# Kernel tuning notes

Measured on AMD Instinct MI355X. Metric: run time of the kernel, lower is better.

The kernel has to match this reference:

```python
import jax, jax.numpy as jnp
import numpy as np

ALPHA = 2.0   # ATan surrogate sharpness (spikingjelly default)
V_TH = 1.0    # spike threshold

@jax.custom_vjp
def spike(v):
    # Heaviside spike at threshold V_TH
    return (v >= V_TH).astype(v.dtype)

def _spike_fwd(v):
    return spike(v), v

def _spike_bwd(v, g):
    # ATan surrogate gradient
    sg = (ALPHA / 2.0) / (1.0 + (jnp.pi / 2.0 * ALPHA * (v - V_TH)) ** 2)
    return (g * sg,)

spike.defvjp(_spike_fwd, _spike_bwd)

N, T, D_IN, HID, D_OUT = 512, 1000, 128, 128, 20

def _linear_params(k, fan_in, fan_out):
    # matches torch nn.Linear default init: U(-1/sqrt(fan_in), 1/sqrt(fan_in))
    s = 1.0 / np.sqrt(fan_in)
    kw, kb = jax.random.split(k)
    W = jax.random.uniform(kw, (fan_out, fan_in), minval=-s, maxval=s, dtype=jnp.float32)
    b = jax.random.uniform(kb, (fan_out,), minval=-s, maxval=s, dtype=jnp.float32)
    return W, b

def setup_inputs() -> dict:
    key = jax.random.key(0)
    kx, k1, k2, k3, k4, k5 = jax.random.split(key, 6)
    x = jax.random.normal(kx, (N, T, D_IN), dtype=jnp.float32)
    Wi1, bi1 = _linear_params(k1, D_IN, HID)   # i2h_1
    Wh1, bh1 = _linear_params(k2, HID, HID)    # h2h_1
    Wi2, bi2 = _linear_params(k3, HID, HID)    # i2h_2
    Wh2, bh2 = _linear_params(k4, HID, HID)    # h2h_2
    Wo,  bo  = _linear_params(k5, HID, D_OUT)  # h2o_2
    return {"x": x, "Wi1": Wi1, "bi1": bi1, "Wh1": Wh1, "bh1": bh1,
            "Wi2": Wi2, "bi2": bi2, "Wh2": Wh2, "bh2": bh2, "Wo": Wo, "bo": bo}

def reference(x, Wi1, bi1, Wh1, bh1, Wi2, bi2, Wh2, bh2, Wo, bo):
    n, t = x.shape[0], x.shape[1]
    s1_0 = jnp.zeros((n, Wh1.shape[0]), dtype=x.dtype)
    s2_0 = jnp.zeros((n, Wh2.shape[0]), dtype=x.dtype)
    acc0 = jnp.zeros((n, Wo.shape[0]), dtype=x.dtype)

    def step(carry, xt):
        s1, s2, acc = carry
        h1 = xt @ Wi1.T + bi1 + s1 @ Wh1.T + bh1
        s1 = spike(h1)
        h2 = s1 @ Wi2.T + bi2 + s2 @ Wh2.T + bh2
        s2 = spike(h2)
        acc = acc + s2 @ Wo.T + bo
        return (s1, s2, acc), None

    # scan over time: x -> [T, N, D_IN]
    (_, _, acc), _ = jax.lax.scan(step, (s1_0, s2_0, acc0), jnp.swapaxes(x, 0, 1))
    return acc / t
```

## Files before the change

### kernel.cpp

```cpp
#include <hip/hip_runtime.h>
#include <cstdint>
#include <cstddef>

#define T_STEPS 1000
#define NS      512
#define HID     128
#define DOUT    20
#define XPAD    129
#define WPAD    129

extern "C" __global__ void __launch_bounds__(512, 1)
srnn_dense(const float* __restrict__ x, const float* __restrict__ Wi1,
           float* __restrict__ D, int t0, int Tc)
{
    extern __shared__ float sm[];
    float* xs = sm;
    float* Wl = sm + 128 * XPAD;
    const int tid = threadIdx.x;
    const int w = tid >> 6, ln = tid & 63;
    const int rb = blockIdx.x * 128;

    for (int i = tid; i < HID * HID / 4; i += 512)
        ((float4*)Wl)[i] = ((const float4*)Wi1)[i];
    for (int i = tid; i < 128 * 32; i += 512) {
        int r = i >> 5, kq = i & 31;
        int cr = rb + r;
        int s = cr / Tc, trel = cr - s * Tc;
        float4 v = ((const float4*)x)[((size_t)s * T_STEPS + t0 + trel) * 32 + kq];
        float* dst = &xs[r * XPAD + 4 * kq];
        dst[0] = v.x; dst[1] = v.y; dst[2] = v.z; dst[3] = v.w;
    }
    __syncthreads();

    const float* xr0 = xs + ln * XPAD;
    const float* xr1 = xs + (64 + ln) * XPAD;
    for (int og = 0; og < 4; ++og) {
        const int o = 16 * w + 4 * og;
        float a[2][4][4];
        #pragma unroll
        for (int r = 0; r < 2; ++r)
            #pragma unroll
            for (int j = 0; j < 4; ++j)
                #pragma unroll
                for (int i = 0; i < 4; ++i) a[r][j][i] = 0.f;

        #pragma unroll 4
        for (int k = 0; k < HID; k += 4) {
            float4 wv[4];
            #pragma unroll
            for (int j = 0; j < 4; ++j)
                wv[j] = *(const float4*)&Wl[(o + j) * HID + k];
            float xa0[4], xa1[4];
            #pragma unroll
            for (int i = 0; i < 4; ++i) { xa0[i] = xr0[k + i]; xa1[i] = xr1[k + i]; }
            #pragma unroll
            for (int j = 0; j < 4; ++j) {
                a[0][j][0] = fmaf(xa0[0], wv[j].x, a[0][j][0]);
                a[0][j][1] = fmaf(xa0[1], wv[j].y, a[0][j][1]);
                a[0][j][2] = fmaf(xa0[2], wv[j].z, a[0][j][2]);
                a[0][j][3] = fmaf(xa0[3], wv[j].w, a[0][j][3]);
                a[1][j][0] = fmaf(xa1[0], wv[j].x, a[1][j][0]);
                a[1][j][1] = fmaf(xa1[1], wv[j].y, a[1][j][1]);
                a[1][j][2] = fmaf(xa1[2], wv[j].z, a[1][j][2]);
                a[1][j][3] = fmaf(xa1[3], wv[j].w, a[1][j][3]);
            }
        }
        #pragma unroll
        for (int r = 0; r < 2; ++r) {
            float4 dv;
            dv.x = (a[r][0][0] + a[r][0][1]) + (a[r][0][2] + a[r][0][3]);
            dv.y = (a[r][1][0] + a[r][1][1]) + (a[r][1][2] + a[r][1][3]);
            dv.z = (a[r][2][0] + a[r][2][1]) + (a[r][2][2] + a[r][2][3]);
            dv.w = (a[r][3][0] + a[r][3][1]) + (a[r][3][2] + a[r][3][3]);
            *(float4*)&D[(size_t)(rb + 64 * r + ln) * HID + o] = dv;
        }
    }
}

extern "C" __global__ void __launch_bounds__(128, 1)
srnn_layer1(const float* __restrict__ D, const float* __restrict__ Wh1,
            const float* __restrict__ bi1, const float* __restrict__ bh1,
            ulonglong2* __restrict__ masks, ulonglong2* __restrict__ state,
            int t0, int Tc, int first)
{
    extern __shared__ float WT[];
    const int tid = threadIdx.x, w = tid >> 6, ln = tid & 63;
    const int s = 2 * blockIdx.x + w;

    for (int i = tid; i < HID * HID / 4; i += 128) {
        int o = i >> 5, jq = i & 31;
        float4 v = ((const float4*)Wh1)[i];
        WT[(4 * jq + 0) * WPAD + o] = v.x; WT[(4 * jq + 1) * WPAD + o] = v.y;
        WT[(4 * jq + 2) * WPAD + o] = v.z; WT[(4 * jq + 3) * WPAD + o] = v.w;
    }
    const float bil = bi1[ln], bih = bi1[64 + ln];
    const float bhl = bh1[ln], bhh = bh1[64 + ln];
    unsigned long long m0 = 0ULL, m1 = 0ULL;
    if (!first) { ulonglong2 st = state[s]; m0 = st.x; m1 = st.y; }

    const float* Drow = D + (size_t)s * Tc * HID;
    float dl[8], dh[8];
    #pragma unroll
    for (int p = 0; p < 8; ++p) {
        int ti = p < Tc ? p : Tc - 1;
        dl[p] = Drow[ti * HID + ln];
        dh[p] = Drow[ti * HID + 64 + ln];
    }
    __syncthreads();

    for (int tt = 0; tt < Tc; tt += 8) {
        #pragma unroll
        for (int u = 0; u < 8; ++u) {
            int t = tt + u;
            if (t >= Tc) break;
            float dense_l = dl[u], dense_h = dh[u];
            int tp = (t + 8 < Tc) ? t + 8 : Tc - 1;
            dl[u] = Drow[tp * HID + ln];
            dh[u] = Drow[tp * HID + 64 + ln];

            float rl = 0.f, rh = 0.f;
            unsigned long long mm = m0;
            while (mm) { int j = __builtin_ctzll(mm); mm &= mm - 1;
                rl += WT[j * WPAD + ln]; rh += WT[j * WPAD + 64 + ln]; }
            mm = m1;
            while (mm) { int j = 64 + __builtin_ctzll(mm); mm &= mm - 1;
                rl += WT[j * WPAD + ln]; rh += WT[j * WPAD + 64 + ln]; }

            float hl = ((dense_l + bil) + rl) + bhl;
            float hh = ((dense_h + bih) + rh) + bhh;
            m0 = __ballot(hl >= 1.0f);
            m1 = __ballot(hh >= 1.0f);
            if (ln == 0) {
                ulonglong2 mv; mv.x = m0; mv.y = m1;
                masks[(size_t)s * T_STEPS + (t0 + t)] = mv;
            }
        }
    }
    if (ln == 0) { ulonglong2 st; st.x = m0; st.y = m1; state[s] = st; }
}

extern "C" __global__ void __launch_bounds__(128, 1)
srnn_layer2(const ulonglong2* __restrict__ masks,
            const float* __restrict__ Wi2, const float* __restrict__ bi2,
            const float* __restrict__ Wh2, const float* __restrict__ bh2,
            const float* __restrict__ Wo,  const float* __restrict__ bo,
            float* __restrict__ out)
{
    extern __shared__ float sm2[];
    float* WI  = sm2;
    float* WH  = sm2 + HID * WPAD;
    float* WOt = sm2 + 2 * HID * WPAD;
    const int tid = threadIdx.x, w = tid >> 6, ln = tid & 63;
    const int s = 2 * blockIdx.x + w;

    for (int i = tid; i < HID * HID / 4; i += 128) {
        int o = i >> 5, jq = i & 31;
        float4 a = ((const float4*)Wi2)[i];
        WI[(4 * jq + 0) * WPAD + o] = a.x; WI[(4 * jq + 1) * WPAD + o] = a.y;
        WI[(4 * jq + 2) * WPAD + o] = a.z; WI[(4 * jq + 3) * WPAD + o] = a.w;
        float4 b = ((const float4*)Wh2)[i];
        WH[(4 * jq + 0) * WPAD + o] = b.x; WH[(4 * jq + 1) * WPAD + o] = b.y;
        WH[(4 * jq + 2) * WPAD + o] = b.z; WH[(4 * jq + 3) * WPAD + o] = b.w;
    }
    for (int i = tid; i < DOUT * HID / 4; i += 128) {
        int o = i >> 5, jq = i & 31;
        float4 v = ((const float4*)Wo)[i];
        WOt[(4 * jq + 0) * DOUT + o] = v.x; WOt[(4 * jq + 1) * DOUT + o] = v.y;
        WOt[(4 * jq + 2) * DOUT + o] = v.z; WOt[(4 * jq + 3) * DOUT + o] = v.w;
    }
    const float bil = bi2[ln], bih = bi2[64 + ln];
    const float bhl = bh2[ln], bhh = bh2[64 + ln];
    const bool  oth = (ln < DOUT);
    const float bol = oth ? bo[ln] : 0.f;

    const ulonglong2* mrow = masks + (size_t)s * T_STEPS;
    ulonglong2 mb[8];
    #pragma unroll
    for (int p = 0; p < 8; ++p) mb[p] = mrow[p];
    unsigned long long p0 = 0ULL, p1 = 0ULL;
    float acc = 0.f;
    __syncthreads();

    for (int tt = 0; tt < T_STEPS; tt += 8) {
        #pragma unroll
        for (int u = 0; u < 8; ++u) {
            int t = tt + u;
            ulonglong2 s1 = mb[u];
            int tp = (t + 8 < T_STEPS) ? t + 8 : T_STEPS - 1;
            mb[u] = mrow[tp];

            float Al = 0.f, Ah = 0.f;
            unsigned long long mm = s1.x;
            while (mm) { int j = __builtin_ctzll(mm); mm &= mm - 1;
                Al += WI[j * WPAD + ln]; Ah += WI[j * WPAD + 64 + ln]; }
            mm = s1.y;
            while (mm) { int j = 64 + __builtin_ctzll(mm); mm &= mm - 1;
                Al += WI[j * WPAD + ln]; Ah += WI[j * WPAD + 64 + ln]; }

            float Bl = 0.f, Bh = 0.f;
            mm = p0;
            while (mm) { int j = __builtin_ctzll(mm); mm &= mm - 1;
                Bl += WH[j * WPAD + ln]; Bh += WH[j * WPAD + 64 + ln]; }
            mm = p1;
            while (mm) { int j = 64 + __builtin_ctzll(mm); mm &= mm - 1;
                Bl += WH[j * WPAD + ln]; Bh += WH[j * WPAD + 64 + ln]; }

            float hl = ((Al + bil) + Bl) + bhl;
            float hh = ((Ah + bih) + Bh) + bhh;
            p0 = __ballot(hl >= 1.0f);
            p1 = __ballot(hh >= 1.0f);

            if (oth) {
                float d = 0.f;
                unsigned long long q = p0;
                while (q) { int j = __builtin_ctzll(q); q &= q - 1; d += WOt[j * DOUT + ln]; }
                q = p1;
                while (q) { int j = 64 + __builtin_ctzll(q); q &= q - 1; d += WOt[j * DOUT + ln]; }
                acc += d;
                acc += bol;
            }
        }
    }
    if (oth) out[s * DOUT + ln] = acc / (float)T_STEPS;
}

extern "C" void kernel_launch(void* const* d_in, const int* in_sizes, int n_in,
                              void* d_out, int out_size, void* d_ws, size_t ws_size,
                              hipStream_t stream) {
    const float* x   = (const float*)d_in[0];
    const float* Wi1 = (const float*)d_in[1];
    const float* bi1 = (const float*)d_in[2];
    const float* Wh1 = (const float*)d_in[3];
    const float* bh1 = (const float*)d_in[4];
    const float* Wi2 = (const float*)d_in[5];
    const float* bi2 = (const float*)d_in[6];
    const float* Wh2 = (const float*)d_in[7];
    const float* bh2 = (const float*)d_in[8];
    const float* Wo  = (const float*)d_in[9];
    const float* bo  = (const float*)d_in[10];
    float* out = (float*)d_out;

    const size_t mask_bytes  = (size_t)NS * T_STEPS * sizeof(ulonglong2);
    const size_t state_bytes = (size_t)NS * sizeof(ulonglong2);
    ulonglong2* masks = (ulonglong2*)d_ws;
    ulonglong2* state = (ulonglong2*)((char*)d_ws + mask_bytes);
    float* D = (float*)((char*)d_ws + mask_bytes + state_bytes);

    size_t avail = ws_size > mask_bytes + state_bytes
                 ? ws_size - mask_bytes - state_bytes : 0;
    const size_t bytes_per_t = (size_t)NS * HID * sizeof(float);
    long tcmax = (long)(avail / bytes_per_t);
    static const int divs[] = {1000, 500, 250, 200, 125, 100, 50, 40, 25, 20, 10, 8, 5, 4, 2, 1};
    int Tc = 1;
    for (int i = 0; i < 16; ++i) if (divs[i] <= tcmax) { Tc = divs[i]; break; }

    const int lds0 = (128 * XPAD + HID * HID) * (int)sizeof(float);
    const int lds1 = (HID * WPAD) * (int)sizeof(float);
    const int lds2 = (2 * HID * WPAD + HID * DOUT) * (int)sizeof(float);
    hipFuncSetAttribute((const void*)srnn_dense,
                        hipFuncAttributeMaxDynamicSharedMemorySize, lds0);
    hipFuncSetAttribute((const void*)srnn_layer1,
                        hipFuncAttributeMaxDynamicSharedMemorySize, lds1);
    hipFuncSetAttribute((const void*)srnn_layer2,
                        hipFuncAttributeMaxDynamicSharedMemorySize, lds2);

    for (int t0 = 0; t0 < T_STEPS; t0 += Tc) {
        srnn_dense<<<4 * Tc, 512, lds0, stream>>>(x, Wi1, D, t0, Tc);
        srnn_layer1<<<NS / 2, 128, lds1, stream>>>(D, Wh1, bi1, bh1, masks, state,
                                                   t0, Tc, t0 == 0 ? 1 : 0);
    }
    srnn_layer2<<<NS / 2, 128, lds2, stream>>>(masks, Wi2, bi2, Wh2, bh2, Wo, bo, out);
}
```

Baseline: 1.766 ms.

## Split layer 2 into parallel sparse input projection, shared recurrence, and output reduction

The serial layer-2 kernel, which did the input projection, recurrence and output dot per time step, is broken into stages. The non-recurrent input projection from layer-1 spikes is computed in parallel across all time steps (srnn_spmm). The layer-1 recurrence kernel is reused for layer 2, and output dots are computed in parallel with a final reduction kernel. The sparse gather loop is also unrolled by four with a zero padding row so that LDS loads can be issued together. This takes non-recurrent work off the sequential critical path, at the cost of extra kernel launches and a larger workspace for masks and dots.

```diff
diff --git a/kernel.cpp b/kernel.cpp
--- a/kernel.cpp
+++ b/kernel.cpp
@@ -77,11 +77,29 @@
     }
 }
 
+__device__ __forceinline__ void sparse4(const float* __restrict__ WT,
+                                        unsigned long long mm, int base,
+                                        int ln, float& rl, float& rh)
+{
+    while (mm) {
+        int j0 = (int)__builtin_ctzll(mm) + base;      mm &= mm - 1;
+        int j1 = mm ? (int)__builtin_ctzll(mm) + base : 128; mm &= mm - 1;
+        int j2 = mm ? (int)__builtin_ctzll(mm) + base : 128; mm &= mm - 1;
+        int j3 = mm ? (int)__builtin_ctzll(mm) + base : 128; mm &= mm - 1;
+        float a0 = WT[j0 * WPAD + ln],      a1 = WT[j1 * WPAD + ln];
+        float a2 = WT[j2 * WPAD + ln],      a3 = WT[j3 * WPAD + ln];
+        float b0 = WT[j0 * WPAD + 64 + ln], b1 = WT[j1 * WPAD + 64 + ln];
+        float b2 = WT[j2 * WPAD + 64 + ln], b3 = WT[j3 * WPAD + 64 + ln];
+        rl += a0; rl += a1; rl += a2; rl += a3;
+        rh += b0; rh += b1; rh += b2; rh += b3;
+    }
+}
+
 extern "C" __global__ void __launch_bounds__(128, 1)
-srnn_layer1(const float* __restrict__ D, const float* __restrict__ Wh1,
-            const float* __restrict__ bi1, const float* __restrict__ bh1,
-            ulonglong2* __restrict__ masks, ulonglong2* __restrict__ state,
-            int t0, int Tc, int first)
+srnn_recur(const float* __restrict__ Dn, const float* __restrict__ Wh,
+           const float* __restrict__ bi, const float* __restrict__ bh,
+           ulonglong2* __restrict__ masks, ulonglong2* __restrict__ state,
+           int t0, int Tc, int first)
 {
     extern __shared__ float WT[];
     const int tid = threadIdx.x, w = tid >> 6, ln = tid & 63;
@@ -89,16 +107,18 @@
 
     for (int i = tid; i < HID * HID / 4; i += 128) {
         int o = i >> 5, jq = i & 31;
-        float4 v = ((const float4*)Wh1)[i];
+        float4 v = ((const float4*)Wh)[i];
         WT[(4 * jq + 0) * WPAD + o] = v.x; WT[(4 * jq + 1) * WPAD + o] = v.y;
         WT[(4 * jq + 2) * WPAD + o] = v.z; WT[(4 * jq + 3) * WPAD + o] = v.w;
     }
-    const float bil = bi1[ln], bih = bi1[64 + ln];
-    const float bhl = bh1[ln], bhh = bh1[64 + ln];
+    for (int i = tid; i < WPAD; i += 128) WT[128 * WPAD + i] = 0.f;
+
+    const float bil = bi[ln], bih = bi[64 + ln];
+    const float bhl = bh[ln], bhh = bh[64 + ln];
     unsigned long long m0 = 0ULL, m1 = 0ULL;
     if (!first) { ulonglong2 st = state[s]; m0 = st.x; m1 = st.y; }
 
-    const float* Drow = D + (size_t)s * Tc * HID;
+    const float* Drow = Dn + (size_t)s * Tc * HID;
     float dl[8], dh[8];
     #pragma unroll
     for (int p = 0; p < 8; ++p) {
@@ -119,12 +139,8 @@
             dh[u] = Drow[tp * HID + 64 + ln];
 
             float rl = 0.f, rh = 0.f;
-            unsigned long long mm = m0;
-            while (mm) { int j = __builtin_ctzll(mm); mm &= mm - 1;
-                rl += WT[j * WPAD + ln]; rh += WT[j * WPAD + 64 + ln]; }
-            mm = m1;
-            while (mm) { int j = 64 + __builtin_ctzll(mm); mm &= mm - 1;
-                rl += WT[j * WPAD + ln]; rh += WT[j * WPAD + 64 + ln]; }
+            sparse4(WT, m0, 0,  ln, rl, rh);
+            sparse4(WT, m1, 64, ln, rl, rh);
 
             float hl = ((dense_l + bil) + rl) + bhl;
             float hh = ((dense_h + bih) + rh) + bhh;
@@ -139,89 +155,78 @@
     if (ln == 0) { ulonglong2 st; st.x = m0; st.y = m1; state[s] = st; }
 }
 
-extern "C" __global__ void __launch_bounds__(128, 1)
-srnn_layer2(const ulonglong2* __restrict__ masks,
-            const float* __restrict__ Wi2, const float* __restrict__ bi2,
-            const float* __restrict__ Wh2, const float* __restrict__ bh2,
-            const float* __restrict__ Wo,  const float* __restrict__ bo,
-            float* __restrict__ out)
-{
-    extern __shared__ float sm2[];
-    float* WI  = sm2;
-    float* WH  = sm2 + HID * WPAD;
-    float* WOt = sm2 + 2 * HID * WPAD;
+extern "C" __global__ void __launch_bounds__(256, 1)
+srnn_spmm(const ulonglong2* __restrict__ masks1, const float* __restrict__ Wi2,
+          float* __restrict__ D2, int t0, int Tc)
+{
+    extern __shared__ float WI[];
     const int tid = threadIdx.x, w = tid >> 6, ln = tid & 63;
-    const int s = 2 * blockIdx.x + w;
-
-    for (int i = tid; i < HID * HID / 4; i += 128) {
+
+    for (int i = tid; i < HID * HID / 4; i += 256) {
         int o = i >> 5, jq = i & 31;
-        float4 a = ((const float4*)Wi2)[i];
-        WI[(4 * jq + 0) * WPAD + o] = a.x; WI[(4 * jq + 1) * WPAD + o] = a.y;
-        WI[(4 * jq + 2) * WPAD + o] = a.z; WI[(4 * jq + 3) * WPAD + o] = a.w;
-        float4 b = ((const float4*)Wh2)[i];
-        WH[(4 * jq + 0) * WPAD + o] = b.x; WH[(4 * jq + 1) * WPAD + o] = b.y;
-        WH[(4 * jq + 2) * WPAD + o] = b.z; WH[(4 * jq + 3) * WPAD + o] = b.w;
-    }
-    for (int i = tid; i < DOUT * HID / 4; i += 128) {
+        float4 v = ((const float4*)Wi2)[i];
+        WI[(4 * jq + 0) * WPAD + o] = v.x; WI[(4 * jq + 1) * WPAD + o] = v.y;
+        WI[(4 * jq + 2) * WPAD + o] = v.z; WI[(4 * jq + 3) * WPAD + o] = v.w;
+    }
+    __syncthreads();
+
+    const int trel = blockIdx.x * 4 + w;
+    const int s = blockIdx.y;
+    if (trel >= Tc) return;
+
+    ulonglong2 m = masks1[(size_t)s * T_STEPS + (t0 + trel)];
+    float Al = 0.f, Ah = 0.f;
+    unsigned long long mm = m.x;
+    while (mm) { int j = __builtin_ctzll(mm); mm &= mm - 1;
+        Al += WI[j * WPAD + ln]; Ah += WI[j * WPAD + 64 + ln]; }
+    mm = m.y;
+    while (mm) { int j = 64 + __builtin_ctzll(mm); mm &= mm - 1;
+        Al += WI[j * WPAD + ln]; Ah += WI[j * WPAD + 64 + ln]; }
+
+    size_t ro = ((size_t)s * Tc + trel) * HID;
+    D2[ro + ln] = Al;
+    D2[ro + 64 + ln] = Ah;
+}
+
+extern "C" __global__ void __launch_bounds__(256, 1)
+srnn_dots(const ulonglong2* __restrict__ masks2, const float* __restrict__ Wo,
+          float* __restrict__ dots)
+{
+    __shared__ float WOt[HID * DOUT];
+    const int tid = threadIdx.x, w = tid >> 6, ln = tid & 63;
+
+    for (int i = tid; i < DOUT * HID / 4; i += 256) {
         int o = i >> 5, jq = i & 31;
         float4 v = ((const float4*)Wo)[i];
         WOt[(4 * jq + 0) * DOUT + o] = v.x; WOt[(4 * jq + 1) * DOUT + o] = v.y;
         WOt[(4 * jq + 2) * DOUT + o] = v.z; WOt[(4 * jq + 3) * DOUT + o] = v.w;
     }
-    const float bil = bi2[ln], bih = bi2[64 + ln];
-    const float bhl = bh2[ln], bhh = bh2[64 + ln];
-    const bool  oth = (ln < DOUT);
-    const float bol = oth ? bo[ln] : 0.f;
-
-    const ulonglong2* mrow = masks + (size_t)s * T_STEPS;
-    ulonglong2 mb[8];
-    #pragma unroll
-    for (int p = 0; p < 8; ++p) mb[p] = mrow[p];
-    unsigned long long p0 = 0ULL, p1 = 0ULL;
+    __syncthreads();
+
+    const int t = blockIdx.x * 4 + w;
+    const int s = blockIdx.y;
+    const int c = ln < DOUT ? ln : 0;
+
+    ulonglong2 q = masks2[(size_t)s * T_STEPS + t];
+    float d = 0.f;
+    unsigned long long mm = q.x;
+    while (mm) { int j = __builtin_ctzll(mm); mm &= mm - 1; d += WOt[j * DOUT + c]; }
+    mm = q.y;
+    while (mm) { int j = 64 + __builtin_ctzll(mm); mm &= mm - 1; d += WOt[j * DOUT + c]; }
+    if (ln < DOUT) dots[((size_t)s * T_STEPS + t) * DOUT + ln] = d;
+}
+
+extern "C" __global__ void __launch_bounds__(256, 1)
+srnn_finish(const float* __restrict__ dots, const float* __restrict__ bo,
+            float* __restrict__ out)
+{
+    const int idx = blockIdx.x * 256 + threadIdx.x;
+    const int s = idx / DOUT, o = idx - s * DOUT;
+    const float bov = bo[o];
+    const float* dp = dots + ((size_t)s * T_STEPS) * DOUT + o;
     float acc = 0.f;
-    __syncthreads();
-
-    for (int tt = 0; tt < T_STEPS; tt += 8) {
-        #pragma unroll
-        for (int u = 0; u < 8; ++u) {
-            int t = tt + u;
-            ulonglong2 s1 = mb[u];
-            int tp = (t + 8 < T_STEPS) ? t + 8 : T_STEPS - 1;
-            mb[u] = mrow[tp];
-
-            float Al = 0.f, Ah = 0.f;
-            unsigned long long mm = s1.x;
-            while (mm) { int j = __builtin_ctzll(mm); mm &= mm - 1;
-                Al += WI[j * WPAD + ln]; Ah += WI[j * WPAD + 64 + ln]; }
-            mm = s1.y;
-            while (mm) { int j = 64 + __builtin_ctzll(mm); mm &= mm - 1;
-                Al += WI[j * WPAD + ln]; Ah += WI[j * WPAD + 64 + ln]; }
-
-            float Bl = 0.f, Bh = 0.f;
-            mm = p0;
-            while (mm) { int j = __builtin_ctzll(mm); mm &= mm - 1;
-                Bl += WH[j * WPAD + ln]; Bh += WH[j * WPAD + 64 + ln]; }
-            mm = p1;
-            while (mm) { int j = 64 + __builtin_ctzll(mm); mm &= mm - 1;
-                Bl += WH[j * WPAD + ln]; Bh += WH[j * WPAD + 64 + ln]; }
-
-            float hl = ((Al + bil) + Bl) + bhl;
-            float hh = ((Ah + bih) + Bh) + bhh;
-            p0 = __ballot(hl >= 1.0f);
-            p1 = __ballot(hh >= 1.0f);
-
-            if (oth) {
-                float d = 0.f;
-                unsigned long long q = p0;
-                while (q) { int j = __builtin_ctzll(q); q &= q - 1; d += WOt[j * DOUT + ln]; }
-                q = p1;
-                while (q) { int j = 64 + __builtin_ctzll(q); q &= q - 1; d += WOt[j * DOUT + ln]; }
-                acc += d;
-                acc += bol;
-            }
-        }
-    }
-    if (oth) out[s * DOUT + ln] = acc / (float)T_STEPS;
+    for (int t = 0; t < T_STEPS; ++t) { acc += dp[t * DOUT]; acc += bov; }
+    out[idx] = acc / (float)T_STEPS;
 }
 
 extern "C" void kernel_launch(void* const* d_in, const int* in_sizes, int n_in,
@@ -240,14 +245,17 @@
     const float* bo  = (const float*)d_in[10];
     float* out = (float*)d_out;
 
-    const size_t mask_bytes  = (size_t)NS * T_STEPS * sizeof(ulonglong2);
-    const size_t state_bytes = (size_t)NS * sizeof(ulonglong2);
-    ulonglong2* masks = (ulonglong2*)d_ws;
-    ulonglong2* state = (ulonglong2*)((char*)d_ws + mask_bytes);
-    float* D = (float*)((char*)d_ws + mask_bytes + state_bytes);
-
-    size_t avail = ws_size > mask_bytes + state_bytes
-                 ? ws_size - mask_bytes - state_bytes : 0;
+    const size_t mb = (size_t)NS * T_STEPS * sizeof(ulonglong2);
+    ulonglong2* masks1 = (ulonglong2*)d_ws;
+    ulonglong2* masks2 = (ulonglong2*)((char*)d_ws + mb);
+    ulonglong2* state  = (ulonglong2*)((char*)d_ws + 2 * mb);
+    const size_t state_bytes = (size_t)2 * NS * sizeof(ulonglong2);
+    float* dots = (float*)((char*)d_ws + 2 * mb + state_bytes);
+    const size_t dots_bytes = (size_t)NS * T_STEPS * DOUT * sizeof(float);
+    float* D = (float*)((char*)d_ws + 2 * mb + state_bytes + dots_bytes);
+
+    const size_t base = 2 * mb + state_bytes + dots_bytes;
+    size_t avail = ws_size > base ? ws_size - base : 0;
     const size_t bytes_per_t = (size_t)NS * HID * sizeof(float);
     long tcmax = (long)(avail / bytes_per_t);
     static const int divs[] = {1000, 500, 250, 200, 125, 100, 50, 40, 25, 20, 10, 8, 5, 4, 2, 1};
@@ -255,19 +263,27 @@
     for (int i = 0; i < 16; ++i) if (divs[i] <= tcmax) { Tc = divs[i]; break; }
 
     const int lds0 = (128 * XPAD + HID * HID) * (int)sizeof(float);
-    const int lds1 = (HID * WPAD) * (int)sizeof(float);
-    const int lds2 = (2 * HID * WPAD + HID * DOUT) * (int)sizeof(float);
+    const int ldsR = (129 * WPAD) * (int)sizeof(float);
+    const int lds2 = (HID * WPAD) * (int)sizeof(float);
     hipFuncSetAttribute((const void*)srnn_dense,
                         hipFuncAttributeMaxDynamicSharedMemorySize, lds0);
-    hipFuncSetAttribute((const void*)srnn_layer1,
-                        hipFuncAttributeMaxDynamicSharedMemorySize, lds1);
-    hipFuncSetAttribute((const void*)srnn_layer2,
+    hipFuncSetAttribute((const void*)srnn_recur,
+                        hipFuncAttributeMaxDynamicSharedMemorySize, ldsR);
+    hipFuncSetAttribute((const void*)srnn_spmm,
                         hipFuncAttributeMaxDynamicSharedMemorySize, lds2);
 
     for (int t0 = 0; t0 < T_STEPS; t0 += Tc) {
         srnn_dense<<<4 * Tc, 512, lds0, stream>>>(x, Wi1, D, t0, Tc);
-        srnn_layer1<<<NS / 2, 128, lds1, stream>>>(D, Wh1, bi1, bh1, masks, state,
-                                                   t0, Tc, t0 == 0 ? 1 : 0);
-    }
-    srnn_layer2<<<NS / 2, 128, lds2, stream>>>(masks, Wi2, bi2, Wh2, bh2, Wo, bo, out);
-}
+        srnn_recur<<<NS / 2, 128, ldsR, stream>>>(D, Wh1, bi1, bh1,
+                                                  masks1, state, t0, Tc, t0 == 0);
+    }
+    for (int t0 = 0; t0 < T_STEPS; t0 += Tc) {
+        dim3 g2((Tc + 3) / 4, NS);
+        srnn_spmm<<<g2, 256, lds2, stream>>>(masks1, Wi2, D, t0, Tc);
+        srnn_recur<<<NS / 2, 128, ldsR, stream>>>(D, Wh2, bi2, bh2,
+                                                  masks2, state + NS, t0, Tc, t0 == 0);
+    }
+    dim3 g4(250, NS);
+    srnn_dots<<<g4, 256, 0, stream>>>(masks2, Wo, dots);
+    srnn_finish<<<40, 256, 0, stream>>>(dots, bo, out);
+}
```

Result: slower. 2.641 ms (+49.6%).
